# Kernel tuning notes

Measured on AMD Instinct MI355X. Metric: run time of the kernel, lower is better.

## Reference

```python
import jax, jax.numpy as jnp
import numpy as np

N, C, H, W = 8, 256, 31, 31
HIDDEN, OUT = 512, 256


def setup_inputs() -> dict:
    key = jax.random.key(0)
    k0, k1, k2, k3, k4 = jax.random.split(key, 5)
    x = jax.random.normal(k0, (N, C, H, W), dtype=jnp.float32)
    # Linear params (torch nn.Linear layout: [out_features, in_features])
    W1 = jax.random.normal(k1, (HIDDEN, C), dtype=jnp.float32) * (1.0 / np.sqrt(C))
    b1 = jax.random.normal(k2, (HIDDEN,), dtype=jnp.float32) * 0.01
    W2 = jax.random.normal(k3, (OUT, HIDDEN), dtype=jnp.float32) * (1.0 / np.sqrt(HIDDEN))
    b2 = jax.random.normal(k4, (OUT,), dtype=jnp.float32) * 0.01
    return {"x": x, "W1": W1, "b1": b1, "W2": W2, "b2": b2}


def _normalized_adjacency(n, h, w):
    M = n * h * w
    idx = jnp.arange(M)
    blk = idx // (h * w)          # sample id of each node
    pos = idx % (h * w)           # spatial position within sample
    # block-diagonal all-ones per sample
    same_block = (blk[:, None] == blk[None, :]).astype(jnp.float32)
    # identity link between consecutive samples (disjoint from block-diag)
    neighbor = ((jnp.abs(blk[:, None] - blk[None, :]) == 1)
                & (pos[:, None] == pos[None, :])).astype(jnp.float32)
    A = same_block + neighbor + jnp.eye(M, dtype=jnp.float32)
    deg = A.sum(axis=1)
    dinv = jnp.where(deg > 0, deg ** -0.5, 0.0)
    return A * dinv[:, None] * dinv[None, :]  # D^-1/2 A D^-1/2


def reference(x, W1, b1, W2, b2):
    n, c, h, w = x.shape
    weight = _normalized_adjacency(n, h, w)                 # [M, M]
    nodes = x.transpose(0, 2, 3, 1).reshape(-1, c)          # [M, C]
    hid = jax.nn.leaky_relu(weight @ nodes @ W1.T + b1)     # [M, HIDDEN]
    hid = jax.nn.leaky_relu(weight @ hid @ W2.T + b2)       # [M, OUT]
    hid = hid.reshape(n, h, w, -1).transpose(0, 3, 1, 2)    # [N, OUT, H, W]
    return hid.max(axis=0, keepdims=True)                   # [1, OUT, H, W]
```

## Files before the change

### kernel.cpp

```cpp
#include <hip/hip_runtime.h>
#include <math.h>

#define NS   8
#define CC   256
#define PP   961
#define MM   7688
#define MP   7744
#define HID  512
#define OUTC 256

typedef _Float16 h16;
using half8   = __attribute__((ext_vector_type(8))) _Float16;
using floatx4 = __attribute__((ext_vector_type(4))) float;

#define AS1 __attribute__((address_space(1)))
#define AS3 __attribute__((address_space(3)))

__device__ __forceinline__ float dinv_of(int b) {
    return (b == 0 || b == NS - 1) ? 0.0322245515f : 0.0322078318f;
}

__device__ __forceinline__ int rho_of(int b, int p) {
    return ((p >> 3) << 6) + (b << 3) + (p & 7);
}

__global__ void prep(const float* __restrict__ W1, const float* __restrict__ W2,
                     h16* __restrict__ w1h, h16* __restrict__ w2h,
                     const float* __restrict__ x, h16* __restrict__ Xt,
                     float* __restrict__ SZ, float* __restrict__ SY) {
    int blk = blockIdx.x, tid = threadIdx.x;
    if (blk < 256) {
        bool second = blk >= 128;
        const float* src = second ? W2 : W1;
        h16* dst = second ? w2h : w1h;
        int i = ((blk & 127) * 256 + tid) * 4;
        float4 v = *(const float4*)(src + i);
        dst[i + 0] = (h16)v.x; dst[i + 1] = (h16)v.y;
        dst[i + 2] = (h16)v.z; dst[i + 3] = (h16)v.w;
    } else if (blk < 2240) {
        __shared__ h16 tr[32][33];
        int t = blk - 256;
        int b = t & 7, ct = (t >> 3) & 7, pt = t >> 6;
        int p0 = pt * 32, c0 = ct * 32;
        int j = tid & 31, i0 = tid >> 5;
        int p = p0 + j;
        #pragma unroll
        for (int r = 0; r < 4; ++r) {
            int c = c0 + i0 + r * 8;
            float v = (p < PP) ? x[((size_t)b * CC + c) * PP + p] : 0.f;
            tr[i0 + r * 8][j] = (h16)v;
        }
        __syncthreads();
        #pragma unroll
        for (int r = 0; r < 4; ++r) {
            int ii = tid & 31;
            int jj = (tid >> 5) + r * 8;
            int pw = p0 + jj;
            if (pw < PP)
                Xt[((size_t)b * PP + pw) * CC + c0 + ii] = tr[ii][jj];
        }
    } else {
        int i = (blk - 2240) * 256 + tid;
        if (i < NS * HID) SZ[i] = 0.f;
        else SY[i - NS * HID] = 0.f;
    }
}

__global__ __launch_bounds__(256) void gemm1(
    const h16* __restrict__ A,
    const h16* __restrict__ B,
    h16* __restrict__ Z,
    float* __restrict__ SZ)
{
    __shared__ __align__(16) h16 As[64 * 64];
    __shared__ __align__(16) h16 Bs[64 * 64];
    int tid = threadIdx.x, wave = tid >> 6, lane = tid & 63;
    int m0 = blockIdx.x * 64, n0 = blockIdx.y * 64;
    int sro = lane >> 3;
    int sch = (lane & 7) ^ sro;
    const h16* ga0 = A + (size_t)(m0 + wave * 16 + sro) * CC + sch * 8;
    const h16* gb0 = B + (size_t)(n0 + wave * 16 + sro) * CC + sch * 8;
    h16* la0 = &As[(wave * 16) * 64];
    h16* la1 = &As[(wave * 16 + 8) * 64];
    h16* lb0 = &Bs[(wave * 16) * 64];
    h16* lb1 = &Bs[(wave * 16 + 8) * 64];
    int fr = lane & 15, fq = lane >> 4;
    floatx4 acc[4] = {{0.f,0.f,0.f,0.f},{0.f,0.f,0.f,0.f},{0.f,0.f,0.f,0.f},{0.f,0.f,0.f,0.f}};
    for (int kk = 0; kk < CC; kk += 64) {
        __builtin_amdgcn_global_load_lds((const AS1 void*)(const void*)(ga0 + kk),
                                         (AS3 void*)(void*)la0, 16, 0, 0);
        __builtin_amdgcn_global_load_lds((const AS1 void*)(const void*)(ga0 + 8 * CC + kk),
                                         (AS3 void*)(void*)la1, 16, 0, 0);
        __builtin_amdgcn_global_load_lds((const AS1 void*)(const void*)(gb0 + kk),
                                         (AS3 void*)(void*)lb0, 16, 0, 0);
        __builtin_amdgcn_global_load_lds((const AS1 void*)(const void*)(gb0 + 8 * CC + kk),
                                         (AS3 void*)(void*)lb1, 16, 0, 0);
        __syncthreads();
        #pragma unroll
        for (int ks = 0; ks < 2; ++ks) {
            int slot = (ks * 4 + fq) ^ (fr & 7);
            half8 bf = *(const half8*)&Bs[(wave * 16 + fr) * 64 + slot * 8];
            #pragma unroll
            for (int mb = 0; mb < 4; ++mb) {
                half8 af = *(const half8*)&As[(mb * 16 + fr) * 64 + slot * 8];
                acc[mb] = __builtin_amdgcn_mfma_f32_16x16x32_f16(af, bf, acc[mb], 0, 0, 0);
            }
        }
        __syncthreads();
    }
    int col = n0 + wave * 16 + fr;
    float s_lo = 0.f, s_hi = 0.f;
    int blo = m0 / 961;
    int mcut = (blo + 1) * 961;
    #pragma unroll
    for (int mb = 0; mb < 4; ++mb) {
        #pragma unroll
        for (int r = 0; r < 4; ++r) {
            int m = m0 + mb * 16 + fq * 4 + r;
            if (m < MM) {
                float v = acc[mb][r];
                int b = m / 961;
                int p = m - b * 961;
                Z[(size_t)rho_of(b, p) * HID + col] = (h16)v;
                if (m < mcut) s_lo += v; else s_hi += v;
            }
        }
    }
    s_lo += __shfl_xor(s_lo, 16);
    s_lo += __shfl_xor(s_lo, 32);
    s_hi += __shfl_xor(s_hi, 16);
    s_hi += __shfl_xor(s_hi, 32);
    if (fq == 0) {
        atomicAdd(&SZ[blo * HID + col], s_lo);
        int bhi = (m0 + 63) / 961;
        if (bhi != blo && bhi < NS) atomicAdd(&SZ[bhi * HID + col], s_hi);
    }
}

__global__ __launch_bounds__(256) void gemm2_rho(
    const h16* __restrict__ Z,
    const h16* __restrict__ B,
    const float* __restrict__ SZ,
    const float* __restrict__ b1v,
    float* __restrict__ Y,
    float* __restrict__ SY)
{
    __shared__ __align__(16) h16 Zs[64 * 64];
    __shared__ __align__(16) h16 Hs[64 * 64];
    __shared__ __align__(16) h16 Bs[64 * 64];
    int tid = threadIdx.x, wave = tid >> 6, lane = tid & 63;
    int rt = blockIdx.x;
    int n0 = blockIdx.y * 64;
    int sro = lane >> 3;
    int sch = (lane & 7) ^ sro;
    const h16* gz0 = Z + (size_t)(rt * 64 + wave * 16 + sro) * HID + sch * 8;
    const h16* gb0 = B + (size_t)(n0 + wave * 16 + sro) * HID + sch * 8;
    h16* lz0 = &Zs[(wave * 16) * 64];
    h16* lz1 = &Zs[(wave * 16 + 8) * 64];
    h16* lb0 = &Bs[(wave * 16) * 64];
    h16* lb1 = &Bs[(wave * 16 + 8) * 64];
    int fr = lane & 15, fq = lane >> 4;
    int hr = tid >> 2;
    int hc0 = (tid & 3) * 2;
    int hb = hr >> 3;
    bool pvalid = (rt * 8 + (hr & 7)) < PP;
    float db  = dinv_of(hb);
    float dmw = (hb > 0)      ? db * dinv_of(hb - 1) : 0.f;
    float dpw = (hb < NS - 1) ? db * dinv_of(hb + 1) : 0.f;
    float db2 = db * db;
    int hrm = (hb > 0)      ? hr - 8 : hr;
    int hrp = (hb < NS - 1) ? hr + 8 : hr;
    floatx4 acc[4] = {{0.f,0.f,0.f,0.f},{0.f,0.f,0.f,0.f},{0.f,0.f,0.f,0.f},{0.f,0.f,0.f,0.f}};
    for (int kk = 0; kk < HID; kk += 64) {
        __builtin_amdgcn_global_load_lds((const AS1 void*)(const void*)(gz0 + kk),
                                         (AS3 void*)(void*)lz0, 16, 0, 0);
        __builtin_amdgcn_global_load_lds((const AS1 void*)(const void*)(gz0 + 8 * HID + kk),
                                         (AS3 void*)(void*)lz1, 16, 0, 0);
        __builtin_amdgcn_global_load_lds((const AS1 void*)(const void*)(gb0 + kk),
                                         (AS3 void*)(void*)lb0, 16, 0, 0);
        __builtin_amdgcn_global_load_lds((const AS1 void*)(const void*)(gb0 + 8 * HID + kk),
                                         (AS3 void*)(void*)lb1, 16, 0, 0);
        __syncthreads();
        #pragma unroll
        for (int qi = 0; qi < 2; ++qi) {
            int ch = hc0 + qi;
            int slot = ch ^ (hr & 7);
            half8 zc = *(const half8*)&Zs[hr  * 64 + slot * 8];
            half8 zm = *(const half8*)&Zs[hrm * 64 + slot * 8];
            half8 zp = *(const half8*)&Zs[hrp * 64 + slot * 8];
            int h0 = kk + ch * 8;
            float4 s0  = *(const float4*)(SZ + hb * HID + h0);
            float4 s1  = *(const float4*)(SZ + hb * HID + h0 + 4);
            float4 bb0 = *(const float4*)(b1v + h0);
            float4 bb1 = *(const float4*)(b1v + h0 + 4);
            float ss[8] = {s0.x, s0.y, s0.z, s0.w, s1.x, s1.y, s1.z, s1.w};
            float bb[8] = {bb0.x, bb0.y, bb0.z, bb0.w, bb1.x, bb1.y, bb1.z, bb1.w};
            half8 o;
            #pragma unroll
            for (int j = 0; j < 8; ++j) {
                float v = db2 * (ss[j] + (float)zc[j])
                        + dmw * (float)zm[j] + dpw * (float)zp[j] + bb[j];
                v = (v >= 0.f) ? v : 0.01f * v;
                o[j] = pvalid ? (h16)v : (h16)0.f;
            }
            *(half8*)&Hs[hr * 64 + slot * 8] = o;
        }
        __syncthreads();
        #pragma unroll
        for (int ks = 0; ks < 2; ++ks) {
            int slot = (ks * 4 + fq) ^ (fr & 7);
            half8 bf = *(const half8*)&Bs[(wave * 16 + fr) * 64 + slot * 8];
            #pragma unroll
            for (int mb = 0; mb < 4; ++mb) {
                half8 af = *(const half8*)&Hs[(mb * 16 + fr) * 64 + slot * 8];
                acc[mb] = __builtin_amdgcn_mfma_f32_16x16x32_f16(af, bf, acc[mb], 0, 0, 0);
            }
        }
        __syncthreads();
    }
    int col = n0 + wave * 16 + fr;
    size_t row0 = (size_t)rt * 64;
    float sb[4];
    #pragma unroll
    for (int mb = 0; mb < 4; ++mb) {
        float s = 0.f;
        #pragma unroll
        for (int r = 0; r < 4; ++r) {
            int row = 16 * mb + 4 * fq + r;
            float v = acc[mb][r];
            Y[(row0 + row) * OUTC + col] = v;
            s += v;
        }
        sb[mb] = s;
    }
    #pragma unroll
    for (int mb = 0; mb < 4; ++mb) sb[mb] += __shfl_xor(sb[mb], 16);
    if (fq == 0 || fq == 2) {
        int bodd = (fq >= 2) ? 1 : 0;
        #pragma unroll
        for (int mb = 0; mb < 4; ++mb)
            atomicAdd(&SY[(2 * mb + bodd) * OUTC + col], sb[mb]);
    }
}

__global__ void final_max(const float* __restrict__ Y, const float* __restrict__ SY,
                          const float* __restrict__ b2, float* __restrict__ out) {
    int pt = blockIdx.x, ot = blockIdx.y;
    int p0 = pt * 32, o0 = ot * 32;
    __shared__ float t[32][33];
    int i = threadIdx.x & 31, j0 = threadIdx.x >> 5;
    int o = o0 + i;
    float bias = b2[o];
    #pragma unroll
    for (int r = 0; r < 4; ++r) {
        int j = j0 + r * 8;
        int p = p0 + j;
        float vmax = -INFINITY;
        if (p < PP) {
            size_t rbase = (size_t)(((p >> 3) << 6) + (p & 7)) * OUTC + o;
            float y[NS];
            #pragma unroll
            for (int b = 0; b < NS; ++b)
                y[b] = Y[rbase + (size_t)b * 8 * OUTC];
            #pragma unroll
            for (int b = 0; b < NS; ++b) {
                float db = dinv_of(b);
                float a = db * (SY[b * OUTC + o] + y[b]);
                if (b > 0)      a += dinv_of(b - 1) * y[b - 1];
                if (b < NS - 1) a += dinv_of(b + 1) * y[b + 1];
                float z = db * a + bias;
                z = (z >= 0.f) ? z : 0.01f * z;
                vmax = fmaxf(vmax, z);
            }
        }
        t[j][i] = vmax;
    }
    __syncthreads();
    int jj = threadIdx.x & 31, ii0 = threadIdx.x >> 5;
    #pragma unroll
    for (int r = 0; r < 4; ++r) {
        int ii = ii0 + r * 8;
        int pw = p0 + jj;
        if (pw < PP)
            out[(size_t)(o0 + ii) * PP + pw] = t[jj][ii];
    }
}

extern "C" void kernel_launch(void* const* d_in, const int* in_sizes, int n_in,
                              void* d_out, int out_size, void* d_ws, size_t ws_size,
                              hipStream_t stream) {
    const float* x  = (const float*)d_in[0];
    const float* W1 = (const float*)d_in[1];
    const float* b1 = (const float*)d_in[2];
    const float* W2 = (const float*)d_in[3];
    const float* b2 = (const float*)d_in[4];
    float* out = (float*)d_out;
    float* ws  = (float*)d_ws;

    float* SZ  = ws;
    float* SY  = ws + 4096;
    h16*  w1h  = (h16*)(ws + 6144);
    h16*  w2h  = (h16*)(ws + 71680);
    h16*  Xt   = (h16*)(ws + 137216);
    h16*  Z    = (h16*)(ws + 1128448);
    float* Y   = ws + 3110912;

    prep<<<2264, 256, 0, stream>>>(W1, W2, w1h, w2h, x, Xt, SZ, SY);
    gemm1<<<dim3(MP / 64, HID / 64), 256, 0, stream>>>(Xt, w1h, Z, SZ);
    gemm2_rho<<<dim3(MP / 64, OUTC / 64), 256, 0, stream>>>(Z, w2h, SZ, b1, Y, SY);
    final_max<<<dim3(31, 8), 256, 0, stream>>>(Y, SY, b2, out);
}
```

Before: 102.8 us.

## Apply graph aggregation before first GEMM using per-sample input sums

Reorders the first layer so the adjacency mix (neighbor and block-sum terms) is applied to the input X (256 channels) before multiplying by W1, rather than to the 512-wide Z afterward. Per-sample column sums of X are computed in prep and projected through W1 in a small new corr kernel, replacing atomics on Z sums. The bias and leaky-relu are fused into the first GEMM epilogue, so the second GEMM becomes a plain GEMM. The cost is an extra kernel launch, and the block-sum correction is now computed from fp16-rounded inputs in fp32.

```diff
diff --git a/kernel.cpp b/kernel.cpp
--- a/kernel.cpp
+++ b/kernel.cpp
@@ -20,14 +20,10 @@
     return (b == 0 || b == NS - 1) ? 0.0322245515f : 0.0322078318f;
 }
 
-__device__ __forceinline__ int rho_of(int b, int p) {
-    return ((p >> 3) << 6) + (b << 3) + (p & 7);
-}
-
 __global__ void prep(const float* __restrict__ W1, const float* __restrict__ W2,
                      h16* __restrict__ w1h, h16* __restrict__ w2h,
                      const float* __restrict__ x, h16* __restrict__ Xt,
-                     float* __restrict__ SZ, float* __restrict__ SY) {
+                     float* __restrict__ S1p, float* __restrict__ SY) {
     int blk = blockIdx.x, tid = threadIdx.x;
     if (blk < 256) {
         bool second = blk >= 128;
@@ -56,163 +52,165 @@
             int ii = tid & 31;
             int jj = (tid >> 5) + r * 8;
             int pw = p0 + jj;
-            if (pw < PP)
-                Xt[((size_t)b * PP + pw) * CC + c0 + ii] = tr[ii][jj];
+            if (pw < PP) {
+                int row = ((pw >> 3) << 6) + (b << 3) + (pw & 7);
+                Xt[(size_t)row * CC + c0 + ii] = tr[ii][jj];
+            }
+        }
+        if (tid < 32) {
+            float s = 0.f;
+            #pragma unroll
+            for (int jj = 0; jj < 32; ++jj) s += (float)tr[tid][jj];
+            S1p[pt * (NS * CC) + b * CC + c0 + tid] = s;
         }
     } else {
-        int i = (blk - 2240) * 256 + tid;
-        if (i < NS * HID) SZ[i] = 0.f;
-        else SY[i - NS * HID] = 0.f;
-    }
-}
-
-__global__ __launch_bounds__(256) void gemm1(
+        for (int i = tid; i < NS * OUTC; i += 256) SY[i] = 0.f;
+    }
+}
+
+__global__ void corr(const float* __restrict__ S1p, const float* __restrict__ W1,
+                     float* __restrict__ SZc) {
+    __shared__ float s1[CC];
+    int b = blockIdx.x >> 2, hq = blockIdx.x & 3;
+    int tid = threadIdx.x;
+    if (tid < CC) {
+        float s = 0.f;
+        for (int pt = 0; pt < 31; ++pt) s += S1p[pt * (NS * CC) + b * CC + tid];
+        s1[tid] = s;
+    }
+    __syncthreads();
+    if (tid < 128) {
+        int h = hq * 128 + tid;
+        const float* wr = W1 + (size_t)h * CC;
+        float dot = 0.f;
+        for (int c = 0; c < CC; c += 4) {
+            float4 w = *(const float4*)(wr + c);
+            dot += s1[c] * w.x + s1[c + 1] * w.y + s1[c + 2] * w.z + s1[c + 3] * w.w;
+        }
+        float db = dinv_of(b);
+        SZc[b * HID + h] = db * db * dot;
+    }
+}
+
+__global__ __launch_bounds__(256) void gemm1_rho(
+    const h16* __restrict__ Xt,
+    const h16* __restrict__ B,
+    const float* __restrict__ SZc,
+    const float* __restrict__ b1v,
+    h16* __restrict__ H1)
+{
+    __shared__ __align__(16) h16 Xs[64 * 64];
+    __shared__ __align__(16) h16 Gs[64 * 64];
+    __shared__ __align__(16) h16 Bs[64 * 64];
+    int tid = threadIdx.x, wave = tid >> 6, lane = tid & 63;
+    int rt = blockIdx.x, n0 = blockIdx.y * 64;
+    int sro = lane >> 3;
+    int sch = (lane & 7) ^ sro;
+    const h16* gx0 = Xt + (size_t)(rt * 64 + wave * 16 + sro) * CC + sch * 8;
+    const h16* gb0 = B + (size_t)(n0 + wave * 16 + sro) * CC + sch * 8;
+    h16* lx0 = &Xs[(wave * 16) * 64];
+    h16* lx1 = &Xs[(wave * 16 + 8) * 64];
+    h16* lb0 = &Bs[(wave * 16) * 64];
+    h16* lb1 = &Bs[(wave * 16 + 8) * 64];
+    int fr = lane & 15, fq = lane >> 4;
+    int hr = tid >> 2, hc0 = (tid & 3) * 2;
+    int hb = hr >> 3;
+    float db  = dinv_of(hb);
+    float db2 = db * db;
+    float dmw = (hb > 0)      ? db * dinv_of(hb - 1) : 0.f;
+    float dpw = (hb < NS - 1) ? db * dinv_of(hb + 1) : 0.f;
+    int hrm = (hb > 0)      ? hr - 8 : hr;
+    int hrp = (hb < NS - 1) ? hr + 8 : hr;
+    floatx4 acc[4] = {{0.f,0.f,0.f,0.f},{0.f,0.f,0.f,0.f},{0.f,0.f,0.f,0.f},{0.f,0.f,0.f,0.f}};
+    for (int kk = 0; kk < CC; kk += 64) {
+        __builtin_amdgcn_global_load_lds((const AS1 void*)(const void*)(gx0 + kk),
+                                         (AS3 void*)(void*)lx0, 16, 0, 0);
+        __builtin_amdgcn_global_load_lds((const AS1 void*)(const void*)(gx0 + 8 * CC + kk),
+                                         (AS3 void*)(void*)lx1, 16, 0, 0);
+        __builtin_amdgcn_global_load_lds((const AS1 void*)(const void*)(gb0 + kk),
+                                         (AS3 void*)(void*)lb0, 16, 0, 0);
+        __builtin_amdgcn_global_load_lds((const AS1 void*)(const void*)(gb0 + 8 * CC + kk),
+                                         (AS3 void*)(void*)lb1, 16, 0, 0);
+        __syncthreads();
+        #pragma unroll
+        for (int qi = 0; qi < 2; ++qi) {
+            int ch = hc0 + qi;
+            int slot = ch ^ (hr & 7);
+            half8 zc = *(const half8*)&Xs[hr  * 64 + slot * 8];
+            half8 zm = *(const half8*)&Xs[hrm * 64 + slot * 8];
+            half8 zp = *(const half8*)&Xs[hrp * 64 + slot * 8];
+            half8 o;
+            #pragma unroll
+            for (int j = 0; j < 8; ++j)
+                o[j] = (h16)(db2 * (float)zc[j] + dmw * (float)zm[j] + dpw * (float)zp[j]);
+            *(half8*)&Gs[hr * 64 + slot * 8] = o;
+        }
+        __syncthreads();
+        #pragma unroll
+        for (int ks = 0; ks < 2; ++ks) {
+            int slot = (ks * 4 + fq) ^ (fr & 7);
+            half8 bf = *(const half8*)&Bs[(wave * 16 + fr) * 64 + slot * 8];
+            #pragma unroll
+            for (int mb = 0; mb < 4; ++mb) {
+                half8 af = *(const half8*)&Gs[(mb * 16 + fr) * 64 + slot * 8];
+                acc[mb] = __builtin_amdgcn_mfma_f32_16x16x32_f16(af, bf, acc[mb], 0, 0, 0);
+            }
+        }
+        __syncthreads();
+    }
+    int col = n0 + wave * 16 + fr;
+    float bv = b1v[col];
+    #pragma unroll
+    for (int mb = 0; mb < 4; ++mb) {
+        #pragma unroll
+        for (int r = 0; r < 4; ++r) {
+            int row = 16 * mb + 4 * fq + r;
+            int b = row >> 3;
+            int p = rt * 8 + (row & 7);
+            float v = acc[mb][r] + SZc[b * HID + col] + bv;
+            v = (v >= 0.f) ? v : 0.01f * v;
+            H1[(size_t)(rt * 64 + row) * HID + col] = (p < PP) ? (h16)v : (h16)0.f;
+        }
+    }
+}
+
+__global__ __launch_bounds__(256) void gemm2_sy(
     const h16* __restrict__ A,
     const h16* __restrict__ B,
-    h16* __restrict__ Z,
-    float* __restrict__ SZ)
+    float* __restrict__ Y,
+    float* __restrict__ SY)
 {
     __shared__ __align__(16) h16 As[64 * 64];
     __shared__ __align__(16) h16 Bs[64 * 64];
     int tid = threadIdx.x, wave = tid >> 6, lane = tid & 63;
-    int m0 = blockIdx.x * 64, n0 = blockIdx.y * 64;
+    int rt = blockIdx.x, n0 = blockIdx.y * 64;
     int sro = lane >> 3;
     int sch = (lane & 7) ^ sro;
-    const h16* ga0 = A + (size_t)(m0 + wave * 16 + sro) * CC + sch * 8;
-    const h16* gb0 = B + (size_t)(n0 + wave * 16 + sro) * CC + sch * 8;
+    const h16* ga0 = A + (size_t)(rt * 64 + wave * 16 + sro) * HID + sch * 8;
+    const h16* gb0 = B + (size_t)(n0 + wave * 16 + sro) * HID + sch * 8;
     h16* la0 = &As[(wave * 16) * 64];
     h16* la1 = &As[(wave * 16 + 8) * 64];
     h16* lb0 = &Bs[(wave * 16) * 64];
     h16* lb1 = &Bs[(wave * 16 + 8) * 64];
     int fr = lane & 15, fq = lane >> 4;
     floatx4 acc[4] = {{0.f,0.f,0.f,0.f},{0.f,0.f,0.f,0.f},{0.f,0.f,0.f,0.f},{0.f,0.f,0.f,0.f}};
-    for (int kk = 0; kk < CC; kk += 64) {
+    for (int kk = 0; kk < HID; kk += 64) {
         __builtin_amdgcn_global_load_lds((const AS1 void*)(const void*)(ga0 + kk),
                                          (AS3 void*)(void*)la0, 16, 0, 0);
-        __builtin_amdgcn_global_load_lds((const AS1 void*)(const void*)(ga0 + 8 * CC + kk),
+        __builtin_amdgcn_global_load_lds((const AS1 void*)(const void*)(ga0 + 8 * HID + kk),
                                          (AS3 void*)(void*)la1, 16, 0, 0);
-        __builtin_amdgcn_global_load_lds((const AS1 void*)(const void*)(gb0 + kk),
-                                         (AS3 void*)(void*)lb0, 16, 0, 0);
-        __builtin_amdgcn_global_load_lds((const AS1 void*)(const void*)(gb0 + 8 * CC + kk),
-                                         (AS3 void*)(void*)lb1, 16, 0, 0);
-        __syncthreads();
-        #pragma unroll
-        for (int ks = 0; ks < 2; ++ks) {
-            int slot = (ks * 4 + fq) ^ (fr & 7);
-            half8 bf = *(const half8*)&Bs[(wave * 16 + fr) * 64 + slot * 8];
-            #pragma unroll
-            for (int mb = 0; mb < 4; ++mb) {
-                half8 af = *(const half8*)&As[(mb * 16 + fr) * 64 + slot * 8];
-                acc[mb] = __builtin_amdgcn_mfma_f32_16x16x32_f16(af, bf, acc[mb], 0, 0, 0);
-            }
-        }
-        __syncthreads();
-    }
-    int col = n0 + wave * 16 + fr;
-    float s_lo = 0.f, s_hi = 0.f;
-    int blo = m0 / 961;
-    int mcut = (blo + 1) * 961;
-    #pragma unroll
-    for (int mb = 0; mb < 4; ++mb) {
-        #pragma unroll
-        for (int r = 0; r < 4; ++r) {
-            int m = m0 + mb * 16 + fq * 4 + r;
-            if (m < MM) {
-                float v = acc[mb][r];
-                int b = m / 961;
-                int p = m - b * 961;
-                Z[(size_t)rho_of(b, p) * HID + col] = (h16)v;
-                if (m < mcut) s_lo += v; else s_hi += v;
-            }
-        }
-    }
-    s_lo += __shfl_xor(s_lo, 16);
-    s_lo += __shfl_xor(s_lo, 32);
-    s_hi += __shfl_xor(s_hi, 16);
-    s_hi += __shfl_xor(s_hi, 32);
-    if (fq == 0) {
-        atomicAdd(&SZ[blo * HID + col], s_lo);
-        int bhi = (m0 + 63) / 961;
-        if (bhi != blo && bhi < NS) atomicAdd(&SZ[bhi * HID + col], s_hi);
-    }
-}
-
-__global__ __launch_bounds__(256) void gemm2_rho(
-    const h16* __restrict__ Z,
-    const h16* __restrict__ B,
-    const float* __restrict__ SZ,
-    const float* __restrict__ b1v,
-    float* __restrict__ Y,
-    float* __restrict__ SY)
-{
-    __shared__ __align__(16) h16 Zs[64 * 64];
-    __shared__ __align__(16) h16 Hs[64 * 64];
-    __shared__ __align__(16) h16 Bs[64 * 64];
-    int tid = threadIdx.x, wave = tid >> 6, lane = tid & 63;
-    int rt = blockIdx.x;
-    int n0 = blockIdx.y * 64;
-    int sro = lane >> 3;
-    int sch = (lane & 7) ^ sro;
-    const h16* gz0 = Z + (size_t)(rt * 64 + wave * 16 + sro) * HID + sch * 8;
-    const h16* gb0 = B + (size_t)(n0 + wave * 16 + sro) * HID + sch * 8;
-    h16* lz0 = &Zs[(wave * 16) * 64];
-    h16* lz1 = &Zs[(wave * 16 + 8) * 64];
-    h16* lb0 = &Bs[(wave * 16) * 64];
-    h16* lb1 = &Bs[(wave * 16 + 8) * 64];
-    int fr = lane & 15, fq = lane >> 4;
-    int hr = tid >> 2;
-    int hc0 = (tid & 3) * 2;
-    int hb = hr >> 3;
-    bool pvalid = (rt * 8 + (hr & 7)) < PP;
-    float db  = dinv_of(hb);
-    float dmw = (hb > 0)      ? db * dinv_of(hb - 1) : 0.f;
-    float dpw = (hb < NS - 1) ? db * dinv_of(hb + 1) : 0.f;
-    float db2 = db * db;
-    int hrm = (hb > 0)      ? hr - 8 : hr;
-    int hrp = (hb < NS - 1) ? hr + 8 : hr;
-    floatx4 acc[4] = {{0.f,0.f,0.f,0.f},{0.f,0.f,0.f,0.f},{0.f,0.f,0.f,0.f},{0.f,0.f,0.f,0.f}};
-    for (int kk = 0; kk < HID; kk += 64) {
-        __builtin_amdgcn_global_load_lds((const AS1 void*)(const void*)(gz0 + kk),
-                                         (AS3 void*)(void*)lz0, 16, 0, 0);
-        __builtin_amdgcn_global_load_lds((const AS1 void*)(const void*)(gz0 + 8 * HID + kk),
-                                         (AS3 void*)(void*)lz1, 16, 0, 0);
         __builtin_amdgcn_global_load_lds((const AS1 void*)(const void*)(gb0 + kk),
                                          (AS3 void*)(void*)lb0, 16, 0, 0);
         __builtin_amdgcn_global_load_lds((const AS1 void*)(const void*)(gb0 + 8 * HID + kk),
                                          (AS3 void*)(void*)lb1, 16, 0, 0);
         __syncthreads();
         #pragma unroll
-        for (int qi = 0; qi < 2; ++qi) {
-            int ch = hc0 + qi;
-            int slot = ch ^ (hr & 7);
-            half8 zc = *(const half8*)&Zs[hr  * 64 + slot * 8];
-            half8 zm = *(const half8*)&Zs[hrm * 64 + slot * 8];
-            half8 zp = *(const half8*)&Zs[hrp * 64 + slot * 8];
-            int h0 = kk + ch * 8;
-            float4 s0  = *(const float4*)(SZ + hb * HID + h0);
-            float4 s1  = *(const float4*)(SZ + hb * HID + h0 + 4);
-            float4 bb0 = *(const float4*)(b1v + h0);
-            float4 bb1 = *(const float4*)(b1v + h0 + 4);
-            float ss[8] = {s0.x, s0.y, s0.z, s0.w, s1.x, s1.y, s1.z, s1.w};
-            float bb[8] = {bb0.x, bb0.y, bb0.z, bb0.w, bb1.x, bb1.y, bb1.z, bb1.w};
-            half8 o;
-            #pragma unroll
-            for (int j = 0; j < 8; ++j) {
-                float v = db2 * (ss[j] + (float)zc[j])
-                        + dmw * (float)zm[j] + dpw * (float)zp[j] + bb[j];
-                v = (v >= 0.f) ? v : 0.01f * v;
-                o[j] = pvalid ? (h16)v : (h16)0.f;
-            }
-            *(half8*)&Hs[hr * 64 + slot * 8] = o;
-        }
-        __syncthreads();
-        #pragma unroll
         for (int ks = 0; ks < 2; ++ks) {
             int slot = (ks * 4 + fq) ^ (fr & 7);
             half8 bf = *(const half8*)&Bs[(wave * 16 + fr) * 64 + slot * 8];
             #pragma unroll
             for (int mb = 0; mb < 4; ++mb) {
-                half8 af = *(const half8*)&Hs[(mb * 16 + fr) * 64 + slot * 8];
+                half8 af = *(const half8*)&As[(mb * 16 + fr) * 64 + slot * 8];
                 acc[mb] = __builtin_amdgcn_mfma_f32_16x16x32_f16(af, bf, acc[mb], 0, 0, 0);
             }
         }
@@ -297,16 +295,18 @@
     float* out = (float*)d_out;
     float* ws  = (float*)d_ws;
 
-    float* SZ  = ws;
-    float* SY  = ws + 4096;
-    h16*  w1h  = (h16*)(ws + 6144);
-    h16*  w2h  = (h16*)(ws + 71680);
-    h16*  Xt   = (h16*)(ws + 137216);
-    h16*  Z    = (h16*)(ws + 1128448);
-    float* Y   = ws + 3110912;
-
-    prep<<<2264, 256, 0, stream>>>(W1, W2, w1h, w2h, x, Xt, SZ, SY);
-    gemm1<<<dim3(MP / 64, HID / 64), 256, 0, stream>>>(Xt, w1h, Z, SZ);
-    gemm2_rho<<<dim3(MP / 64, OUTC / 64), 256, 0, stream>>>(Z, w2h, SZ, b1, Y, SY);
+    float* S1p = ws;
+    float* SZc = ws + 63488;
+    float* SY  = ws + 67584;
+    h16*  w1h  = (h16*)(ws + 69632);
+    h16*  w2h  = (h16*)(ws + 135168);
+    h16*  Xt   = (h16*)(ws + 200704);
+    h16*  H1   = (h16*)(ws + 1191936);
+    float* Y   = ws + 3174400;
+
+    prep<<<2241, 256, 0, stream>>>(W1, W2, w1h, w2h, x, Xt, S1p, SY);
+    corr<<<32, 256, 0, stream>>>(S1p, W1, SZc);
+    gemm1_rho<<<dim3(MP / 64, HID / 64), 256, 0, stream>>>(Xt, w1h, SZc, b1, H1);
+    gemm2_sy<<<dim3(MP / 64, OUTC / 64), 256, 0, stream>>>(H1, w2h, Y, SY);
     final_max<<<dim3(31, 8), 256, 0, stream>>>(Y, SY, b2, out);
 }
```

Measured after the change: 103.5 us. No clear change (+0.7%).
